# Optimization experiments

Hardware: AMD Instinct MI355X
Metric: run time of the kernel (lower is better)

The kernel has to match this reference:

```python
import jax, jax.numpy as jnp
import numpy as np

D_MODEL = 1024
D_FF = 4096
N_EXPERTS = 8
TOP_K = 2
AUX_COEF = 0.01
ZLOSS_COEF = 0.001
EPS = 1e-9


def setup_inputs() -> dict:
    key = jax.random.key(0)
    k0, k1, k2, k3 = jax.random.split(key, 4)
    x = jax.random.normal(k0, (4, 2048, D_MODEL), dtype=jnp.float32)
    router_w = jax.random.normal(k1, (N_EXPERTS, D_MODEL), dtype=jnp.float32) * 0.02
    w1 = jax.random.normal(k2, (N_EXPERTS, D_FF, D_MODEL), dtype=jnp.float32) * 0.02
    b1 = jnp.zeros((N_EXPERTS, D_FF), dtype=jnp.float32)
    w2 = jax.random.normal(k3, (N_EXPERTS, D_MODEL, D_FF), dtype=jnp.float32) * 0.02
    b2 = jnp.zeros((N_EXPERTS, D_MODEL), dtype=jnp.float32)
    return {"x": x, "router_w": router_w, "w1": w1, "b1": b1, "w2": w2, "b2": b2}


def reference(x, router_w, w1, b1, w2, b2):
    B, T, D = x.shape
    N = B * T
    xf = x.reshape(N, D)

    # Router: logits [N, E], softmax probs, top-k selection + renormalized weights
    logits = jnp.einsum('nd,ed->ne', xf, router_w)
    probs = jax.nn.softmax(logits, axis=-1)
    topk_vals, topk_idx = jax.lax.top_k(probs, TOP_K)  # [N, K]
    topk_w = topk_vals / (topk_vals.sum(axis=-1, keepdims=True) + EPS)

    # Dense combine weights [N, E] (top-k indices are unique per row)
    combine = jnp.zeros((N, N_EXPERTS), dtype=xf.dtype)
    combine = combine.at[jnp.arange(N)[:, None], topk_idx].add(topk_w)

    # Per-expert MLP (fixed small loop over experts), weighted combine.
    # drop_tokens=False => no capacity truncation; masked-dense == gather/scatter math.
    y = jnp.zeros_like(xf)
    for e in range(N_EXPERTS):
        h = jax.nn.gelu(jnp.einsum('nd,fd->nf', xf, w1[e]) + b1[e], approximate=False)
        out_e = jnp.einsum('nf,df->nd', h, w2[e]) + b2[e]
        y = y + out_e * combine[:, e:e + 1]

    # Aux losses / stats
    importance = probs.sum(axis=0)                                   # [E]
    expert_load = jnp.zeros((N_EXPERTS,), jnp.float32).at[topk_idx.reshape(-1)].add(1.0)
    imp_n = importance / (importance.sum() + EPS)
    load_n = expert_load / (expert_load.sum() + EPS)
    balance_loss = N_EXPERTS * jnp.sum(imp_n * load_n)
    z_loss = jnp.mean(jax.nn.logsumexp(logits, axis=-1) ** 2)
    aux_loss = AUX_COEF * balance_loss + ZLOSS_COEF * z_loss

    return y.reshape(B, T, D), aux_loss, expert_load, importance
```

## Files before the change

kernel.cpp:

```cpp
#include <hip/hip_runtime.h>
#include <math.h>

#define NTOK 8192
#define DMODEL 1024
#define DFF 4096
#define NEXP 8
#define TILE 128
#define MAXTILES 136
#define MAXROWS (MAXTILES * TILE)
#define MOE_EPS 1e-9f
#define REG 4096

typedef unsigned short u16;
typedef __bf16 bf16x8 __attribute__((ext_vector_type(8)));
typedef float f32x4 __attribute__((ext_vector_type(4)));

struct Ctrl {
    int counts[NEXP];
    int fill[NEXP];
    int padded_off[NEXP];
    int n_tiles;
    int tile_expert[MAXTILES];
    int tile_base[MAXTILES];
    int tile_valid[MAXTILES];
    float imp[NEXP];
    float zacc;
};

__device__ __forceinline__ u16 f2bf(float f) {
    unsigned u = __float_as_uint(f);
    unsigned r = u + 0x7fffu + ((u >> 16) & 1u);
    return (u16)(r >> 16);
}

__device__ __forceinline__ void load16(const void* g, void* l) {
    __builtin_amdgcn_global_load_lds((__attribute__((address_space(1))) void*)g,
                                     (__attribute__((address_space(3))) void*)l,
                                     16, 0, 0);
}

__device__ __forceinline__ float gelu_fast(float h) {
    float u = h * (1.5957691216f + 0.0713548162f * h * h);
    return h / (1.f + __expf(-u));
}

__global__ __launch_bounds__(256) void k_convert(const float* __restrict__ src,
                                                 u16* __restrict__ dst, int n4) {
    int i = blockIdx.x * 256 + threadIdx.x;
    int stride = gridDim.x * 256;
    for (; i < n4; i += stride) {
        float4 v = ((const float4*)src)[i];
        ushort4 o;
        o.x = f2bf(v.x); o.y = f2bf(v.y); o.z = f2bf(v.z); o.w = f2bf(v.w);
        ((ushort4*)dst)[i] = o;
    }
}

__global__ __launch_bounds__(256) void k_router(const float* __restrict__ x,
                                                const float* __restrict__ rw,
                                                u16* __restrict__ xb,
                                                int* __restrict__ top_idx,
                                                float* __restrict__ top_w,
                                                Ctrl* __restrict__ ctrl) {
    __shared__ float srw[NEXP * DMODEL];
    __shared__ float simp[NEXP];
    __shared__ float szl;
    int tid = threadIdx.x;
    for (int i = tid; i < NEXP * DMODEL / 4; i += 256)
        ((float4*)srw)[i] = ((const float4*)rw)[i];
    if (tid < NEXP) simp[tid] = 0.f;
    if (tid == 0) szl = 0.f;
    __syncthreads();

    int lane = tid & 63;
    int n = blockIdx.x * 4 + (tid >> 6);
    float p[NEXP];
#pragma unroll
    for (int e = 0; e < NEXP; ++e) p[e] = 0.f;
    const float4* xr = (const float4*)(x + (size_t)n * DMODEL);
    u16 xs[16];
#pragma unroll
    for (int j = 0; j < 4; ++j) {
        float4 xv = xr[lane * 4 + j];
        int d = (lane * 4 + j) * 4;
        xs[j * 4 + 0] = f2bf(xv.x);
        xs[j * 4 + 1] = f2bf(xv.y);
        xs[j * 4 + 2] = f2bf(xv.z);
        xs[j * 4 + 3] = f2bf(xv.w);
#pragma unroll
        for (int e = 0; e < NEXP; ++e) {
            const float* r = srw + e * DMODEL + d;
            p[e] += xv.x * r[0] + xv.y * r[1] + xv.z * r[2] + xv.w * r[3];
        }
    }
    {
        uint4* dst = (uint4*)(xb + (size_t)n * DMODEL + lane * 16);
        dst[0] = ((const uint4*)xs)[0];
        dst[1] = ((const uint4*)xs)[1];
    }
#pragma unroll
    for (int e = 0; e < NEXP; ++e) {
#pragma unroll
        for (int off = 32; off > 0; off >>= 1) p[e] += __shfl_xor(p[e], off);
    }
    if (lane == 0) {
        float m = p[0];
#pragma unroll
        for (int e = 1; e < NEXP; ++e) m = fmaxf(m, p[e]);
        float pr[NEXP];
        float s = 0.f;
#pragma unroll
        for (int e = 0; e < NEXP; ++e) { pr[e] = expf(p[e] - m); s += pr[e]; }
        float inv = 1.f / s;
#pragma unroll
        for (int e = 0; e < NEXP; ++e) pr[e] *= inv;
        float lse = m + logf(s);
        int i0 = 0; float v0 = pr[0];
#pragma unroll
        for (int e = 1; e < NEXP; ++e) if (pr[e] > v0) { v0 = pr[e]; i0 = e; }
        int i1 = -1; float v1 = -1.f;
#pragma unroll
        for (int e = 0; e < NEXP; ++e) if (e != i0 && pr[e] > v1) { v1 = pr[e]; i1 = e; }
        float den = v0 + v1 + MOE_EPS;
        top_idx[n * 2] = i0;
        top_idx[n * 2 + 1] = i1;
        top_w[n * 2] = v0 / den;
        top_w[n * 2 + 1] = v1 / den;
#pragma unroll
        for (int e = 0; e < NEXP; ++e) atomicAdd(&simp[e], pr[e]);
        atomicAdd(&szl, lse * lse);
    }
    __syncthreads();
    if (tid < NEXP) atomicAdd(&ctrl->imp[tid], simp[tid]);
    if (tid == 255) atomicAdd(&ctrl->zacc, szl);
}

__global__ __launch_bounds__(256) void k_build(const int* __restrict__ top_idx,
                                               Ctrl* __restrict__ ctrl,
                                               int* __restrict__ tok_idx,
                                               float* __restrict__ tok_w) {
    __shared__ int cnt[NEXP];
    __shared__ int off[NEXP];
    __shared__ int tiles[NEXP];
    int tid = threadIdx.x;
    if (tid < NEXP) cnt[tid] = 0;
    __syncthreads();
    for (int i = tid; i < NTOK * 2; i += 256) atomicAdd(&cnt[top_idx[i]], 1);
    __syncthreads();
    if (tid == 0) {
        int o = 0, t = 0;
        for (int e = 0; e < NEXP; ++e) {
            int c = cnt[e];
            int te = (c + TILE - 1) / TILE;
            ctrl->counts[e] = c;
            ctrl->padded_off[e] = o;
            off[e] = o;
            tiles[e] = te;
            for (int i = 0; i < te; ++i) {
                ctrl->tile_expert[t] = e;
                ctrl->tile_base[t] = o + i * TILE;
                int v = c - i * TILE;
                ctrl->tile_valid[t] = v > TILE ? TILE : v;
                ++t;
            }
            o += te * TILE;
        }
        ctrl->n_tiles = t;
    }
    __syncthreads();
    for (int e = 0; e < NEXP; ++e) {
        int start = off[e] + cnt[e];
        int end = off[e] + tiles[e] * TILE;
        for (int i = start + tid; i < end; i += 256) {
            tok_idx[i] = 0;
            tok_w[i] = 0.f;
        }
    }
}

__global__ __launch_bounds__(256) void k_fill(const int* __restrict__ top_idx,
                                              const float* __restrict__ top_w,
                                              Ctrl* __restrict__ ctrl,
                                              int* __restrict__ tok_idx,
                                              float* __restrict__ tok_w) {
    int n = blockIdx.x * 256 + threadIdx.x;
    if (n >= NTOK) return;
#pragma unroll
    for (int k = 0; k < 2; ++k) {
        int e = top_idx[n * 2 + k];
        int pos = atomicAdd(&ctrl->fill[e], 1);
        int slot = ctrl->padded_off[e] + pos;
        tok_idx[slot] = n;
        tok_w[slot] = top_w[n * 2 + k];
    }
}

#define KLOOP2(STA, STB, NK)                                                          \
    STA(0, 0, 0); STB(0, 0, 0);                                                       \
    STA(0, 0, 1); STB(0, 0, 1);                                                       \
    STA(1, 1, 0); STB(1, 1, 0);                                                       \
    asm volatile("s_waitcnt vmcnt(8)" ::: "memory");                                  \
    __builtin_amdgcn_s_barrier();                                                     \
    for (int kt = 0; kt < (NK); ++kt) {                                               \
        int p = kt & 1;                                                               \
        const u16* Ar; const u16* Br;                                                 \
        bf16x8 a[4], b[4];                                                            \
                                                              \
        Ar = sA + (p * 2 + 0) * REG; Br = sB + (p * 2 + 0) * REG;                     \
        _Pragma("unroll") for (int m = 0; m < 4; ++m) a[m] = *(const bf16x8*)(Ar + aoff[m]); \
        _Pragma("unroll") for (int n = 0; n < 4; ++n) b[n] = *(const bf16x8*)(Br + boff[n]); \
        if (kt + 1 < (NK)) { STA(p ^ 1, kt + 1, 1); STB(p ^ 1, kt + 1, 1); }          \
        __builtin_amdgcn_s_setprio(1);                                                \
        _Pragma("unroll") for (int m = 0; m < 4; ++m)                                 \
            _Pragma("unroll") for (int n = 0; n < 4; ++n)                             \
                acc[m][n] = __builtin_amdgcn_mfma_f32_16x16x32_bf16(a[m], b[n], acc[m][n], 0, 0, 0); \
        __builtin_amdgcn_s_setprio(0);                                                \
        if (kt == (NK) - 1) asm volatile("s_waitcnt vmcnt(0)" ::: "memory");          \
        else                asm volatile("s_waitcnt vmcnt(8)" ::: "memory");          \
        __builtin_amdgcn_s_barrier();                                                 \
                                                              \
        Ar = sA + (p * 2 + 1) * REG; Br = sB + (p * 2 + 1) * REG;                     \
        _Pragma("unroll") for (int m = 0; m < 4; ++m) a[m] = *(const bf16x8*)(Ar + aoff[m]); \
        _Pragma("unroll") for (int n = 0; n < 4; ++n) b[n] = *(const bf16x8*)(Br + boff[n]); \
        if (kt + 2 < (NK)) { STA(p, kt + 2, 0); STB(p, kt + 2, 0); }                  \
        __builtin_amdgcn_s_setprio(1);                                                \
        _Pragma("unroll") for (int m = 0; m < 4; ++m)                                 \
            _Pragma("unroll") for (int n = 0; n < 4; ++n)                             \
                acc[m][n] = __builtin_amdgcn_mfma_f32_16x16x32_bf16(a[m], b[n], acc[m][n], 0, 0, 0); \
        __builtin_amdgcn_s_setprio(0);                                                \
        if (kt < (NK) - 1) {                                                          \
            if (kt < (NK) - 2) asm volatile("s_waitcnt vmcnt(8)" ::: "memory");       \
            else               asm volatile("s_waitcnt vmcnt(4)" ::: "memory");       \
            __builtin_amdgcn_s_barrier();                                             \
        }                                                                             \
    }

__global__ __launch_bounds__(256, 2) void k_gemm1(const u16* __restrict__ xb,
                                                  const u16* __restrict__ w1b,
                                                  const float* __restrict__ b1,
                                                  const int* __restrict__ tok_idx,
                                                  const Ctrl* __restrict__ ctrl,
                                                  u16* __restrict__ H) {
    int flat = blockIdx.x;
    int t = (flat & 7) + ((flat >> 8) << 3);
    int n0 = ((flat >> 3) & 31) * TILE;
    if (t >= ctrl->n_tiles) return;
    int e = ctrl->tile_expert[t];
    int rbase = ctrl->tile_base[t];

    __shared__ __align__(16) u16 sA[2 * 2 * REG];
    __shared__ __align__(16) u16 sB[2 * 2 * REG];

    int tid = threadIdx.x;
    const u16* aS[2];
    const u16* bS[2];
    int fo[2];
#pragma unroll
    for (int q = 0; q < 2; ++q) {
        int f = q * 256 + tid;
        int row = f >> 2;
        int lc = (f & 3) ^ ((row >> 1) & 3);
        aS[q] = xb + (size_t)tok_idx[rbase + row] * DMODEL + lc * 8;
        bS[q] = w1b + (size_t)e * DFF * DMODEL + (size_t)(n0 + row) * DMODEL + lc * 8;
        fo[q] = f * 8;
    }

#define STA1(pp, kt, h)                                                               \
    do { _Pragma("unroll") for (int q = 0; q < 2; ++q)                                \
        load16(aS[q] + (kt) * 64 + (h) * 32, &sA[((pp) * 2 + (h)) * REG + fo[q]]); } while (0)
#define STB1(pp, kt, h)                                                               \
    do { _Pragma("unroll") for (int q = 0; q < 2; ++q)                                \
        load16(bS[q] + (kt) * 64 + (h) * 32, &sB[((pp) * 2 + (h)) * REG + fo[q]]); } while (0)

    int lane = tid & 63, w = tid >> 6;
    int wr = w >> 1, wc = w & 1;
    int l15 = lane & 15, lg = lane >> 4;
    int csw = (lg ^ ((l15 >> 1) & 3)) * 8;

    int aoff[4], boff[4];
#pragma unroll
    for (int m = 0; m < 4; ++m) aoff[m] = (wr * 64 + m * 16 + l15) * 32 + csw;
#pragma unroll
    for (int n = 0; n < 4; ++n) boff[n] = (wc * 64 + n * 16 + l15) * 32 + csw;

    f32x4 acc[4][4];
#pragma unroll
    for (int m = 0; m < 4; ++m)
#pragma unroll
        for (int n = 0; n < 4; ++n) acc[m][n] = (f32x4){0.f, 0.f, 0.f, 0.f};

    KLOOP2(STA1, STB1, DMODEL / 64)
#undef STA1
#undef STB1

    float bias[4];
#pragma unroll
    for (int n = 0; n < 4; ++n) bias[n] = b1[e * DFF + n0 + wc * 64 + n * 16 + l15];
#pragma unroll
    for (int m = 0; m < 4; ++m)
#pragma unroll
        for (int n = 0; n < 4; ++n) {
            int gcol = n0 + wc * 64 + n * 16 + l15;
#pragma unroll
            for (int r = 0; r < 4; ++r) {
                int grow = wr * 64 + m * 16 + lg * 4 + r;
                float h = acc[m][n][r] + bias[n];
                H[(size_t)(rbase + grow) * DFF + gcol] = f2bf(gelu_fast(h));
            }
        }
}

__global__ __launch_bounds__(256, 2) void k_gemm2(const u16* __restrict__ H,
                                                  const u16* __restrict__ w2b,
                                                  const float* __restrict__ b2,
                                                  const int* __restrict__ tok_idx,
                                                  const float* __restrict__ tok_w,
                                                  const Ctrl* __restrict__ ctrl,
                                                  float* __restrict__ y) {
    int flat = blockIdx.x;
    int t = (flat & 7) + ((flat >> 6) << 3);
    int n0 = ((flat >> 3) & 7) * TILE;
    if (t >= ctrl->n_tiles) return;
    int e = ctrl->tile_expert[t];
    int rbase = ctrl->tile_base[t];
    int valid = ctrl->tile_valid[t];

    __shared__ __align__(16) u16 sA[2 * 2 * REG];
    __shared__ __align__(16) u16 sB[2 * 2 * REG];

    int tid = threadIdx.x;
    const u16* aS[2];
    const u16* bS[2];
    int fo[2];
#pragma unroll
    for (int q = 0; q < 2; ++q) {
        int f = q * 256 + tid;
        int row = f >> 2;
        int lc = (f & 3) ^ ((row >> 1) & 3);
        aS[q] = H + (size_t)(rbase + row) * DFF + lc * 8;
        bS[q] = w2b + (size_t)e * DMODEL * DFF + (size_t)(n0 + row) * DFF + lc * 8;
        fo[q] = f * 8;
    }

#define STA2(pp, kt, h)                                                               \
    do { _Pragma("unroll") for (int q = 0; q < 2; ++q)                                \
        load16(aS[q] + (kt) * 64 + (h) * 32, &sA[((pp) * 2 + (h)) * REG + fo[q]]); } while (0)
#define STB2(pp, kt, h)                                                               \
    do { _Pragma("unroll") for (int q = 0; q < 2; ++q)                                \
        load16(bS[q] + (kt) * 64 + (h) * 32, &sB[((pp) * 2 + (h)) * REG + fo[q]]); } while (0)

    int lane = tid & 63, w = tid >> 6;
    int wr = w >> 1, wc = w & 1;
    int l15 = lane & 15, lg = lane >> 4;
    int csw = (lg ^ ((l15 >> 1) & 3)) * 8;

    int aoff[4], boff[4];
#pragma unroll
    for (int m = 0; m < 4; ++m) aoff[m] = (wr * 64 + m * 16 + l15) * 32 + csw;
#pragma unroll
    for (int n = 0; n < 4; ++n) boff[n] = (wc * 64 + n * 16 + l15) * 32 + csw;

    f32x4 acc[4][4];
#pragma unroll
    for (int m = 0; m < 4; ++m)
#pragma unroll
        for (int n = 0; n < 4; ++n) acc[m][n] = (f32x4){0.f, 0.f, 0.f, 0.f};

    KLOOP2(STA2, STB2, DFF / 64)
#undef STA2
#undef STB2

    float bias[4];
#pragma unroll
    for (int n = 0; n < 4; ++n) bias[n] = b2[e * DMODEL + n0 + wc * 64 + n * 16 + l15];
#pragma unroll
    for (int m = 0; m < 4; ++m)
#pragma unroll
        for (int n = 0; n < 4; ++n) {
            int gcol = n0 + wc * 64 + n * 16 + l15;
#pragma unroll
            for (int r = 0; r < 4; ++r) {
                int grow = wr * 64 + m * 16 + lg * 4 + r;
                if (grow < valid) {
                    int slot = rbase + grow;
                    int tok = tok_idx[slot];
                    float wgt = tok_w[slot];
                    unsafeAtomicAdd(&y[(size_t)tok * DMODEL + gcol],
                                    wgt * (acc[m][n][r] + bias[n]));
                }
            }
        }
}

__global__ void k_final(const Ctrl* __restrict__ ctrl, float* __restrict__ out) {
    if (blockIdx.x == 0 && threadIdx.x == 0) {
        float imp[NEXP], ld[NEXP];
        float imps = 0.f, loads = 0.f;
        for (int e = 0; e < NEXP; ++e) {
            imp[e] = ctrl->imp[e];
            ld[e] = (float)ctrl->counts[e];
            imps += imp[e];
            loads += ld[e];
        }
        float bal = 0.f;
        for (int e = 0; e < NEXP; ++e)
            bal += (imp[e] / (imps + MOE_EPS)) * (ld[e] / (loads + MOE_EPS));
        bal *= (float)NEXP;
        float z = ctrl->zacc / (float)NTOK;
        float aux = 0.01f * bal + 0.001f * z;
        size_t base = (size_t)NTOK * DMODEL;
        out[base] = aux;
        for (int e = 0; e < NEXP; ++e) out[base + 1 + e] = ld[e];
        for (int e = 0; e < NEXP; ++e) out[base + 9 + e] = imp[e];
    }
}

extern "C" void kernel_launch(void* const* d_in, const int* in_sizes, int n_in,
                              void* d_out, int out_size, void* d_ws, size_t ws_size,
                              hipStream_t stream) {
    (void)in_sizes; (void)n_in; (void)out_size; (void)ws_size;
    const float* x  = (const float*)d_in[0];
    const float* rw = (const float*)d_in[1];
    const float* w1 = (const float*)d_in[2];
    const float* b1 = (const float*)d_in[3];
    const float* w2 = (const float*)d_in[4];
    const float* b2 = (const float*)d_in[5];
    float* out = (float*)d_out;

    char* p = (char*)d_ws;
    Ctrl* ctrl = (Ctrl*)p;          p += 4096;
    u16* xb    = (u16*)p;           p += (size_t)NTOK * DMODEL * 2;
    u16* w1b   = (u16*)p;           p += (size_t)NEXP * DFF * DMODEL * 2;
    u16* w2b   = (u16*)p;           p += (size_t)NEXP * DMODEL * DFF * 2;
    u16* Hbuf  = (u16*)p;           p += (size_t)MAXROWS * DFF * 2;
    int* tok_idx = (int*)p;         p += (size_t)MAXROWS * 4;
    float* tok_w = (float*)p;       p += (size_t)MAXROWS * 4;
    int* tIdx  = (int*)p;           p += (size_t)NTOK * 2 * 4;
    float* tW  = (float*)p;         p += (size_t)NTOK * 2 * 4;

    hipMemsetAsync(ctrl, 0, sizeof(Ctrl), stream);
    hipMemsetAsync(d_out, 0, (size_t)NTOK * DMODEL * sizeof(float), stream);

    k_convert<<<2048, 256, 0, stream>>>(w1, w1b, NEXP * DFF * DMODEL / 4);
    k_convert<<<2048, 256, 0, stream>>>(w2, w2b, NEXP * DMODEL * DFF / 4);

    k_router<<<NTOK / 4, 256, 0, stream>>>(x, rw, xb, tIdx, tW, ctrl);
    k_build<<<1, 256, 0, stream>>>(tIdx, ctrl, tok_idx, tok_w);
    k_fill<<<NTOK / 256, 256, 0, stream>>>(tIdx, tW, ctrl, tok_idx, tok_w);

    k_gemm1<<<MAXTILES * (DFF / TILE), 256, 0, stream>>>(xb, w1b, b1, tok_idx, ctrl, Hbuf);
    k_gemm2<<<MAXTILES * (DMODEL / TILE), 256, 0, stream>>>(Hbuf, w2b, b2, tok_idx, tok_w, ctrl, out);

    k_final<<<1, 64, 0, stream>>>(ctrl, out);
}
```

Baseline: 806.5 us.

## Shrink GEMM k-step to 32 with two-stage LDS buffer and higher occupancy

Replaces the four-region, half-step prefetch pipeline with a simpler double buffer of 32-wide k slices. Each iteration waits, reads fragments from LDS, runs the MFMAs, then prefetches two steps ahead. LDS per block is halved and launch bounds go from 2 to 4 blocks per CU, so more waves can hide memory latency. The cost is twice as many barriers per unit of K and less prefetch depth per block, and four blocks per CU may strain registers given the 64-float accumulator.

New measurement: 750.5 us. 6.9% less time.

```diff
diff --git a/kernel.cpp b/kernel.cpp
--- a/kernel.cpp
+++ b/kernel.cpp
@@ -195,47 +195,29 @@
     }
 }
 
-#define KLOOP2(STA, STB, NK)                                                          \
-    STA(0, 0, 0); STB(0, 0, 0);                                                       \
-    STA(0, 0, 1); STB(0, 0, 1);                                                       \
-    STA(1, 1, 0); STB(1, 1, 0);                                                       \
-    asm volatile("s_waitcnt vmcnt(8)" ::: "memory");                                  \
-    __builtin_amdgcn_s_barrier();                                                     \
+#define KLOOP3(STA, STB, NK)                                                          \
+    STA(0, 0); STB(0, 0);                                                             \
+    STA(1, 1); STB(1, 1);                                                             \
     for (int kt = 0; kt < (NK); ++kt) {                                               \
         int p = kt & 1;                                                               \
-        const u16* Ar; const u16* Br;                                                 \
+        if (kt < (NK) - 1) asm volatile("s_waitcnt vmcnt(4)" ::: "memory");           \
+        else               asm volatile("s_waitcnt vmcnt(0)" ::: "memory");           \
+        __builtin_amdgcn_s_barrier();                                                 \
+        const u16* Ar = sA + p * REG;                                                 \
+        const u16* Br = sB + p * REG;                                                 \
         bf16x8 a[4], b[4];                                                            \
-                                                              \
-        Ar = sA + (p * 2 + 0) * REG; Br = sB + (p * 2 + 0) * REG;                     \
         _Pragma("unroll") for (int m = 0; m < 4; ++m) a[m] = *(const bf16x8*)(Ar + aoff[m]); \
         _Pragma("unroll") for (int n = 0; n < 4; ++n) b[n] = *(const bf16x8*)(Br + boff[n]); \
-        if (kt + 1 < (NK)) { STA(p ^ 1, kt + 1, 1); STB(p ^ 1, kt + 1, 1); }          \
         __builtin_amdgcn_s_setprio(1);                                                \
         _Pragma("unroll") for (int m = 0; m < 4; ++m)                                 \
             _Pragma("unroll") for (int n = 0; n < 4; ++n)                             \
                 acc[m][n] = __builtin_amdgcn_mfma_f32_16x16x32_bf16(a[m], b[n], acc[m][n], 0, 0, 0); \
         __builtin_amdgcn_s_setprio(0);                                                \
-        if (kt == (NK) - 1) asm volatile("s_waitcnt vmcnt(0)" ::: "memory");          \
-        else                asm volatile("s_waitcnt vmcnt(8)" ::: "memory");          \
         __builtin_amdgcn_s_barrier();                                                 \
-                                                              \
-        Ar = sA + (p * 2 + 1) * REG; Br = sB + (p * 2 + 1) * REG;                     \
-        _Pragma("unroll") for (int m = 0; m < 4; ++m) a[m] = *(const bf16x8*)(Ar + aoff[m]); \
-        _Pragma("unroll") for (int n = 0; n < 4; ++n) b[n] = *(const bf16x8*)(Br + boff[n]); \
-        if (kt + 2 < (NK)) { STA(p, kt + 2, 0); STB(p, kt + 2, 0); }                  \
-        __builtin_amdgcn_s_setprio(1);                                                \
-        _Pragma("unroll") for (int m = 0; m < 4; ++m)                                 \
-            _Pragma("unroll") for (int n = 0; n < 4; ++n)                             \
-                acc[m][n] = __builtin_amdgcn_mfma_f32_16x16x32_bf16(a[m], b[n], acc[m][n], 0, 0, 0); \
-        __builtin_amdgcn_s_setprio(0);                                                \
-        if (kt < (NK) - 1) {                                                          \
-            if (kt < (NK) - 2) asm volatile("s_waitcnt vmcnt(8)" ::: "memory");       \
-            else               asm volatile("s_waitcnt vmcnt(4)" ::: "memory");       \
-            __builtin_amdgcn_s_barrier();                                             \
-        }                                                                             \
-    }
-
-__global__ __launch_bounds__(256, 2) void k_gemm1(const u16* __restrict__ xb,
+        if (kt + 2 < (NK)) { STA(p, kt + 2); STB(p, kt + 2); }                        \
+    }
+
+__global__ __launch_bounds__(256, 4) void k_gemm1(const u16* __restrict__ xb,
                                                   const u16* __restrict__ w1b,
                                                   const float* __restrict__ b1,
                                                   const int* __restrict__ tok_idx,
@@ -248,8 +230,8 @@
     int e = ctrl->tile_expert[t];
     int rbase = ctrl->tile_base[t];
 
-    __shared__ __align__(16) u16 sA[2 * 2 * REG];
-    __shared__ __align__(16) u16 sB[2 * 2 * REG];
+    __shared__ __align__(16) u16 sA[2 * REG];
+    __shared__ __align__(16) u16 sB[2 * REG];
 
     int tid = threadIdx.x;
     const u16* aS[2];
@@ -265,12 +247,12 @@
         fo[q] = f * 8;
     }
 
-#define STA1(pp, kt, h)                                                               \
+#define STA1(pp, kt)                                                                  \
     do { _Pragma("unroll") for (int q = 0; q < 2; ++q)                                \
-        load16(aS[q] + (kt) * 64 + (h) * 32, &sA[((pp) * 2 + (h)) * REG + fo[q]]); } while (0)
-#define STB1(pp, kt, h)                                                               \
+        load16(aS[q] + (kt) * 32, &sA[(pp) * REG + fo[q]]); } while (0)
+#define STB1(pp, kt)                                                                  \
     do { _Pragma("unroll") for (int q = 0; q < 2; ++q)                                \
-        load16(bS[q] + (kt) * 64 + (h) * 32, &sB[((pp) * 2 + (h)) * REG + fo[q]]); } while (0)
+        load16(bS[q] + (kt) * 32, &sB[(pp) * REG + fo[q]]); } while (0)
 
     int lane = tid & 63, w = tid >> 6;
     int wr = w >> 1, wc = w & 1;
@@ -289,7 +271,7 @@
 #pragma unroll
         for (int n = 0; n < 4; ++n) acc[m][n] = (f32x4){0.f, 0.f, 0.f, 0.f};
 
-    KLOOP2(STA1, STB1, DMODEL / 64)
+    KLOOP3(STA1, STB1, DMODEL / 32)
 #undef STA1
 #undef STB1
 
@@ -310,7 +292,7 @@
         }
 }
 
-__global__ __launch_bounds__(256, 2) void k_gemm2(const u16* __restrict__ H,
+__global__ __launch_bounds__(256, 4) void k_gemm2(const u16* __restrict__ H,
                                                   const u16* __restrict__ w2b,
                                                   const float* __restrict__ b2,
                                                   const int* __restrict__ tok_idx,
@@ -325,8 +307,8 @@
     int rbase = ctrl->tile_base[t];
     int valid = ctrl->tile_valid[t];
 
-    __shared__ __align__(16) u16 sA[2 * 2 * REG];
-    __shared__ __align__(16) u16 sB[2 * 2 * REG];
+    __shared__ __align__(16) u16 sA[2 * REG];
+    __shared__ __align__(16) u16 sB[2 * REG];
 
     int tid = threadIdx.x;
     const u16* aS[2];
@@ -342,12 +324,12 @@
         fo[q] = f * 8;
     }
 
-#define STA2(pp, kt, h)                                                               \
+#define STA2(pp, kt)                                                                  \
     do { _Pragma("unroll") for (int q = 0; q < 2; ++q)                                \
-        load16(aS[q] + (kt) * 64 + (h) * 32, &sA[((pp) * 2 + (h)) * REG + fo[q]]); } while (0)
-#define STB2(pp, kt, h)                                                               \
+        load16(aS[q] + (kt) * 32, &sA[(pp) * REG + fo[q]]); } while (0)
+#define STB2(pp, kt)                                                                  \
     do { _Pragma("unroll") for (int q = 0; q < 2; ++q)                                \
-        load16(bS[q] + (kt) * 64 + (h) * 32, &sB[((pp) * 2 + (h)) * REG + fo[q]]); } while (0)
+        load16(bS[q] + (kt) * 32, &sB[(pp) * REG + fo[q]]); } while (0)
 
     int lane = tid & 63, w = tid >> 6;
     int wr = w >> 1, wc = w & 1;
@@ -366,7 +348,7 @@
 #pragma unroll
         for (int n = 0; n < 4; ++n) acc[m][n] = (f32x4){0.f, 0.f, 0.f, 0.f};
 
-    KLOOP2(STA2, STB2, DFF / 64)
+    KLOOP3(STA2, STB2, DFF / 32)
 #undef STA2
 #undef STB2
 
```
